# Performance work log

Measured on AMD Instinct MI355X. Metric: run time of the kernel, lower is better.

The kernel has to match this reference:

```python
import jax, jax.numpy as jnp
import numpy as np

B, T, I, H = 64, 2048, 128, 256


def setup_inputs() -> dict:
    key = jax.random.key(0)
    k1, k2, k3 = jax.random.split(key, 3)
    inputs = jax.random.normal(k1, (B, T, I), dtype=jnp.float32)
    # 4 gates (input, forget, context, output), each an affine op on [x_t, h]
    W_x = jax.random.normal(k2, (4, I, H), dtype=jnp.float32) * (1.0 / np.sqrt(I))
    W_h = jax.random.normal(k3, (4, H, H), dtype=jnp.float32) * (1.0 / np.sqrt(H))
    b = jnp.zeros((4, H), dtype=jnp.float32)
    return {"inputs": inputs, "W_x": W_x, "W_h": W_h, "b": b}


def reference(inputs, W_x, W_h, b):
    # inputs: [B, T, I]; W_x: [4, I, H]; W_h: [4, H, H]; b: [4, H]
    Bb = inputs.shape[0]
    Hh = W_h.shape[-1]
    h0 = jnp.zeros((Bb, Hh), dtype=inputs.dtype)
    c0 = jnp.zeros((Bb, Hh), dtype=inputs.dtype)

    def step(carry, x_t):
        h, c = carry
        # all 4 gate pre-activations at once: [4, B, H]
        g = (jnp.einsum('bi,gih->gbh', x_t, W_x)
             + jnp.einsum('bh,ghk->gbk', h, W_h)
             + b[:, None, :])
        i_gate = jax.nn.sigmoid(g[0])
        f_gate = jax.nn.sigmoid(g[1])
        g_gate = jnp.tanh(g[2])
        o_gate = jax.nn.sigmoid(g[3])
        c_new = f_gate * c + i_gate * g_gate
        h_new = o_gate * jnp.tanh(c_new)
        return (h_new, c_new), h_new

    xs = jnp.swapaxes(inputs, 0, 1)  # [T, B, I]
    (_, _), hs = jax.lax.scan(step, (h0, c0), xs)  # hs: [T, B, H]
    return jnp.swapaxes(hs, 0, 1)  # [B, T, H]
```

## Files before the change

kernel.cpp:

```cpp
#include <hip/hip_runtime.h>
#include <hip/hip_bf16.h>


#define B_ 64
#define T_ 2048
#define I_ 128
#define H_ 256
#define NC 1024

typedef __attribute__((ext_vector_type(8))) short bf16x8;
typedef __attribute__((ext_vector_type(4))) float f32x4;

static __device__ __forceinline__ unsigned short f2bf(float f) {
    unsigned u = __builtin_bit_cast(unsigned, f);
    u = (u + 0x7FFFu + ((u >> 16) & 1u)) >> 16;
    return (unsigned short)u;
}

static __device__ __forceinline__ int dot4(unsigned a, unsigned b, int c) {
#if __has_builtin(__builtin_amdgcn_sdot4)
    return __builtin_amdgcn_sdot4((int)a, (int)b, c, false);
#else
    int r = c;
    r += (int)(signed char)(a) * (int)(signed char)(b);
    r += (int)(signed char)(a >> 8) * (int)(signed char)(b >> 8);
    r += (int)(signed char)(a >> 16) * (int)(signed char)(b >> 16);
    r += (int)(signed char)(a >> 24) * (int)(signed char)(b >> 24);
    return r;
#endif
}

static __device__ __forceinline__ float fastrcp(float x) {
    return __builtin_amdgcn_rcpf(x);
}

__global__ void pack_wh(const float* __restrict__ Wh, unsigned* __restrict__ wq,
                        float* __restrict__ sws) {
    int col = blockIdx.x;
    int g = col >> 8, j = col & 255;
    int lane = threadIdx.x;
    float v[4];
    float m = 0.f;
#pragma unroll
    for (int u = 0; u < 4; ++u) {
        int k = lane * 4 + u;
        v[u] = Wh[(g * H_ + k) * H_ + j];
        m = fmaxf(m, fabsf(v[u]));
    }
#pragma unroll
    for (int off = 32; off; off >>= 1) m = fmaxf(m, __shfl_xor(m, off));
    float mm = (m > 0.f) ? m : 1.f;
    float inv = 127.f / mm;
    unsigned pack = 0;
#pragma unroll
    for (int u = 0; u < 4; ++u) {
        int q = (int)rintf(v[u] * inv);
        q = max(-127, min(127, q));
        pack |= ((unsigned)(q & 255)) << (8 * u);
    }
    wq[col * 64 + lane] = pack;
    if (lane == 0) sws[col] = mm / (127.f * 127.f);
}

__global__ void pack_wx(const float* __restrict__ Wx,
                        unsigned short* __restrict__ bxp) {
    int f = blockIdx.x * blockDim.x + threadIdx.x;
    int j = f & 7;
    int col = (f >> 3) & 1023;
    int c16 = f >> 13;
    int k = (c16 >> 2) * 32 + (c16 & 3) * 8 + j;
    int g = col >> 8, h = col & 255;
    bxp[f] = f2bf(Wx[(g * I_ + k) * H_ + h]);
}

__global__ __launch_bounds__(256) void gemm_gx(
    const float* __restrict__ A, const unsigned short* __restrict__ Bp,
    unsigned short* __restrict__ Cg) {
    __shared__ uint4 sm[4096];
    int tid = threadIdx.x;
    int mt = blockIdx.x, nt = blockIdx.y;

    const float* Ab = A + (size_t)mt * 128 * I_;
    unsigned* dstA = (unsigned*)sm;
#pragma unroll
    for (int it = 0; it < 16; ++it) {
        int flat = it * 1024 + tid * 4;
        float4 a4 = *(const float4*)(Ab + flat);
        int m = flat >> 7, k0 = flat & 127;
        int c16 = k0 >> 3, j0 = k0 & 7;
        unsigned lo = (unsigned)f2bf(a4.x) | ((unsigned)f2bf(a4.y) << 16);
        unsigned hi = (unsigned)f2bf(a4.z) | ((unsigned)f2bf(a4.w) << 16);
        int didx = ((c16 * 128 + m) * 16 + j0 * 2) >> 2;
        dstA[didx] = lo;
        dstA[didx + 1] = hi;
    }
    const uint4* Bq = (const uint4*)Bp;
#pragma unroll
    for (int it = 0; it < 8; ++it) {
        int chunk = it * 2 + (tid >> 7);
        int inner = tid & 127;
        sm[2048 + chunk * 128 + inner] = Bq[chunk * 1024 + nt * 128 + inner];
    }
    __syncthreads();

    int wid = tid >> 6, lane = tid & 63;
    int r = lane & 15, q = lane >> 4;
    int mw = (wid & 1) * 64, nw = (wid >> 1) * 64;
    f32x4 acc[4][4] = {};
#pragma unroll
    for (int ki = 0; ki < 4; ++ki) {
        bf16x8 af[4], bfr[4];
#pragma unroll
        for (int x = 0; x < 4; ++x) {
            af[x] = __builtin_bit_cast(bf16x8,
                                       sm[(ki * 4 + q) * 128 + mw + x * 16 + r]);
            bfr[x] = __builtin_bit_cast(
                bf16x8, sm[2048 + (ki * 4 + q) * 128 + nw + x * 16 + r]);
        }
#pragma unroll
        for (int x = 0; x < 4; ++x)
#pragma unroll
            for (int y = 0; y < 4; ++y)
                acc[x][y] = __builtin_amdgcn_mfma_f32_16x16x32_bf16(
                    af[x], bfr[y], acc[x][y], 0, 0, 0);
    }
    __syncthreads();

    _Float16* ct = (_Float16*)sm;
#pragma unroll
    for (int x = 0; x < 4; ++x)
#pragma unroll
        for (int y = 0; y < 4; ++y)
#pragma unroll
            for (int g2 = 0; g2 < 4; ++g2) {
                int row = mw + x * 16 + q * 4 + g2;
                int colc = nw + y * 16 + r;
                ct[row * 128 + colc] = (_Float16)acc[x][y][g2];
            }
    __syncthreads();
    int m = tid >> 1, half = tid & 1;
    const uint4* src = (const uint4*)sm;
    uint4* dstg =
        (uint4*)(Cg + ((size_t)(mt * 128 + m) * NC + nt * 128 + half * 64));
#pragma unroll
    for (int i = 0; i < 8; ++i) dstg[i] = src[m * 16 + half * 8 + i];
}

__global__ __launch_bounds__(1024, 4) void lstm_rec(
    const unsigned short* __restrict__ gx, const uint4* __restrict__ wq4,
    const float* __restrict__ sws, const float* __restrict__ bias,
    float* __restrict__ out) {
    int b = blockIdx.x, tid = threadIdx.x;
    int w = tid >> 6;
    int lane = tid & 63;
    int g = lane >> 4;
    int jj = lane & 15;
    int j = w * 16 + jj;
    int col = g * H_ + j;

    uint4 wv[16];
#pragma unroll
    for (int i = 0; i < 16; ++i) wv[i] = wq4[col * 16 + i];
    float sc = sws[col];
    float bb = bias[col];

    __shared__ uint4 hq[2][16];
    if (tid < 16) hq[0][tid] = (uint4){0u, 0u, 0u, 0u};
    __syncthreads();

    float c = 0.f;
    const _Float16* gxh = (const _Float16*)gx;
    size_t rowbase = (size_t)b * T_;
    float gxv = (float)gxh[rowbase * NC + col];

    for (int t = 0; t < T_; ++t) {
        size_t row = rowbase + t;
        size_t prow = rowbase + ((t < T_ - 1) ? (t + 1) : t);
        float nxv = (float)gxh[prow * NC + col];

        const uint4* hb = hq[t & 1];
        int a0 = 0, a1 = 0, a2 = 0, a3 = 0;
#pragma unroll
        for (int ib = 0; ib < 4; ++ib) {
            uint4 h0 = hb[ib * 4 + 0], h1 = hb[ib * 4 + 1];
            uint4 h2 = hb[ib * 4 + 2], h3 = hb[ib * 4 + 3];
            uint4 w0 = wv[ib * 4 + 0], w1 = wv[ib * 4 + 1];
            uint4 w2 = wv[ib * 4 + 2], w3 = wv[ib * 4 + 3];
            a0 = dot4(w0.x, h0.x, a0); a0 = dot4(w0.y, h0.y, a0);
            a0 = dot4(w0.z, h0.z, a0); a0 = dot4(w0.w, h0.w, a0);
            a1 = dot4(w1.x, h1.x, a1); a1 = dot4(w1.y, h1.y, a1);
            a1 = dot4(w1.z, h1.z, a1); a1 = dot4(w1.w, h1.w, a1);
            a2 = dot4(w2.x, h2.x, a2); a2 = dot4(w2.y, h2.y, a2);
            a2 = dot4(w2.z, h2.z, a2); a2 = dot4(w2.w, h2.w, a2);
            a3 = dot4(w3.x, h3.x, a3); a3 = dot4(w3.y, h3.y, a3);
            a3 = dot4(w3.z, h3.z, a3); a3 = dot4(w3.w, h3.w, a3);
        }
        float gpre = (float)((a0 + a1) + (a2 + a3)) * sc + gxv + bb;

        bool isg = (g == 2);
        float arg = isg ? (-2.f * gpre) : (-gpre);
        float e = __expf(arg);
        float r = fastrcp(1.f + e);
        float v = isg ? (2.f * r - 1.f) : r;

        float fv = __shfl(v, jj + 16, 64);
        float gv = __shfl(v, jj + 32, 64);
        float ov = __shfl(v, jj + 48, 64);

        if (g == 0) {
            c = fv * c + v * gv;
            float ec = __expf(-2.f * c);
            float th = 2.f * fastrcp(1.f + ec) - 1.f;
            float h = ov * th;
            out[row * H_ + j] = h;
            int qv = (int)rintf(h * 127.f);
            ((signed char*)hq[(t + 1) & 1])[j] = (signed char)qv;
        }
        __syncthreads();

        gxv = nxv;
    }
}

extern "C" void kernel_launch(void* const* d_in, const int* in_sizes, int n_in,
                              void* d_out, int out_size, void* d_ws,
                              size_t ws_size, hipStream_t stream) {
    const float* inputs = (const float*)d_in[0];
    const float* Wx = (const float*)d_in[1];
    const float* Wh = (const float*)d_in[2];
    const float* bias = (const float*)d_in[3];
    float* out = (float*)d_out;

    char* ws = (char*)d_ws;
    unsigned short* gxbuf = (unsigned short*)ws;
    size_t off = (size_t)B_ * T_ * NC * 2;
    unsigned* wq = (unsigned*)(ws + off);
    off += (size_t)NC * 64 * 4;
    float* sws = (float*)(ws + off);
    off += (size_t)NC * 4;
    unsigned short* bxp = (unsigned short*)(ws + off);
    off += (size_t)I_ * NC * 2;

    pack_wh<<<NC, 64, 0, stream>>>(Wh, wq, sws);
    pack_wx<<<(I_ * NC) / 256, 256, 0, stream>>>(Wx, bxp);
    gemm_gx<<<dim3((B_ * T_) / 128, NC / 128), 256, 0, stream>>>(inputs, bxp,
                                                                 gxbuf);
    lstm_rec<<<B_, 1024, 0, stream>>>(gxbuf, (const uint4*)wq, sws, bias, out);
}
```

Before: 2.292 ms.

## Compute recurrent int8 matvec with MFMA i8 instructions instead of sdot4

Repacks the quantized recurrent weights into the MFMA A-fragment layout. Each wave now computes its four gates' 16 hidden units with 16x16x64 int8 MFMAs, with the h vector broadcast as the B operand. Results are extracted from column 0 through a per-wave LDS scratch and read back per lane. This replaces 64 scalar dot4 ops per lane per step with a few matrix instructions, at the cost of redundant columns and an extra LDS round trip on the serial critical path.

```diff
diff --git a/kernel.cpp b/kernel.cpp
--- a/kernel.cpp
+++ b/kernel.cpp
@@ -10,6 +10,7 @@
 
 typedef __attribute__((ext_vector_type(8))) short bf16x8;
 typedef __attribute__((ext_vector_type(4))) float f32x4;
+typedef __attribute__((ext_vector_type(4))) int i32x4;
 
 static __device__ __forceinline__ unsigned short f2bf(float f) {
     unsigned u = __builtin_bit_cast(unsigned, f);
@@ -17,24 +18,11 @@
     return (unsigned short)u;
 }
 
-static __device__ __forceinline__ int dot4(unsigned a, unsigned b, int c) {
-#if __has_builtin(__builtin_amdgcn_sdot4)
-    return __builtin_amdgcn_sdot4((int)a, (int)b, c, false);
-#else
-    int r = c;
-    r += (int)(signed char)(a) * (int)(signed char)(b);
-    r += (int)(signed char)(a >> 8) * (int)(signed char)(b >> 8);
-    r += (int)(signed char)(a >> 16) * (int)(signed char)(b >> 16);
-    r += (int)(signed char)(a >> 24) * (int)(signed char)(b >> 24);
-    return r;
-#endif
-}
-
 static __device__ __forceinline__ float fastrcp(float x) {
     return __builtin_amdgcn_rcpf(x);
 }
 
-__global__ void pack_wh(const float* __restrict__ Wh, unsigned* __restrict__ wq,
+__global__ void pack_wh(const float* __restrict__ Wh, unsigned* __restrict__ afr,
                         float* __restrict__ sws) {
     int col = blockIdx.x;
     int g = col >> 8, j = col & 255;
@@ -58,7 +46,10 @@
         q = max(-127, min(127, q));
         pack |= ((unsigned)(q & 255)) << (8 * u);
     }
-    wq[col * 64 + lane] = pack;
+    int fragid = ((j >> 4) * 4 + g) * 4 + (lane >> 4);
+    int fl = (((lane & 15) >> 2) * 16) + (j & 15);
+    int didx = (fragid * 64 + fl) * 4 + (lane & 3);
+    afr[didx] = pack;
     if (lane == 0) sws[col] = mm / (127.f * 127.f);
 }
 
@@ -147,7 +138,7 @@
 }
 
 __global__ __launch_bounds__(1024, 4) void lstm_rec(
-    const unsigned short* __restrict__ gx, const uint4* __restrict__ wq4,
+    const unsigned short* __restrict__ gx, const uint4* __restrict__ afr,
     const float* __restrict__ sws, const float* __restrict__ bias,
     float* __restrict__ out) {
     int b = blockIdx.x, tid = threadIdx.x;
@@ -158,13 +149,18 @@
     int j = w * 16 + jj;
     int col = g * H_ + j;
 
-    uint4 wv[16];
-#pragma unroll
-    for (int i = 0; i < 16; ++i) wv[i] = wq4[col * 16 + i];
+    uint4 af[4][4];
+#pragma unroll
+    for (int gg = 0; gg < 4; ++gg)
+#pragma unroll
+        for (int kt = 0; kt < 4; ++kt)
+            af[gg][kt] = afr[(((w * 4 + gg) * 4) + kt) * 64 + lane];
+
     float sc = sws[col];
     float bb = bias[col];
 
     __shared__ uint4 hq[2][16];
+    __shared__ __align__(16) int sg[16 * 64];
     if (tid < 16) hq[0][tid] = (uint4){0u, 0u, 0u, 0u};
     __syncthreads();
 
@@ -178,24 +174,32 @@
         size_t prow = rowbase + ((t < T_ - 1) ? (t + 1) : t);
         float nxv = (float)gxh[prow * NC + col];
 
-        const uint4* hb = hq[t & 1];
-        int a0 = 0, a1 = 0, a2 = 0, a3 = 0;
-#pragma unroll
-        for (int ib = 0; ib < 4; ++ib) {
-            uint4 h0 = hb[ib * 4 + 0], h1 = hb[ib * 4 + 1];
-            uint4 h2 = hb[ib * 4 + 2], h3 = hb[ib * 4 + 3];
-            uint4 w0 = wv[ib * 4 + 0], w1 = wv[ib * 4 + 1];
-            uint4 w2 = wv[ib * 4 + 2], w3 = wv[ib * 4 + 3];
-            a0 = dot4(w0.x, h0.x, a0); a0 = dot4(w0.y, h0.y, a0);
-            a0 = dot4(w0.z, h0.z, a0); a0 = dot4(w0.w, h0.w, a0);
-            a1 = dot4(w1.x, h1.x, a1); a1 = dot4(w1.y, h1.y, a1);
-            a1 = dot4(w1.z, h1.z, a1); a1 = dot4(w1.w, h1.w, a1);
-            a2 = dot4(w2.x, h2.x, a2); a2 = dot4(w2.y, h2.y, a2);
-            a2 = dot4(w2.z, h2.z, a2); a2 = dot4(w2.w, h2.w, a2);
-            a3 = dot4(w3.x, h3.x, a3); a3 = dot4(w3.y, h3.y, a3);
-            a3 = dot4(w3.z, h3.z, a3); a3 = dot4(w3.w, h3.w, a3);
-        }
-        float gpre = (float)((a0 + a1) + (a2 + a3)) * sc + gxv + bb;
+        const char* hb = (const char*)hq[t & 1];
+        i32x4 d0 = {0, 0, 0, 0}, d1 = {0, 0, 0, 0};
+        i32x4 d2 = {0, 0, 0, 0}, d3 = {0, 0, 0, 0};
+#pragma unroll
+        for (int kt = 0; kt < 4; ++kt) {
+            uint4 bf = *(const uint4*)(hb + kt * 64 + ((lane >> 4) << 4));
+            i32x4 bfi = __builtin_bit_cast(i32x4, bf);
+            d0 = __builtin_amdgcn_mfma_i32_16x16x64_i8(
+                __builtin_bit_cast(i32x4, af[0][kt]), bfi, d0, 0, 0, 0);
+            d1 = __builtin_amdgcn_mfma_i32_16x16x64_i8(
+                __builtin_bit_cast(i32x4, af[1][kt]), bfi, d1, 0, 0, 0);
+            d2 = __builtin_amdgcn_mfma_i32_16x16x64_i8(
+                __builtin_bit_cast(i32x4, af[2][kt]), bfi, d2, 0, 0, 0);
+            d3 = __builtin_amdgcn_mfma_i32_16x16x64_i8(
+                __builtin_bit_cast(i32x4, af[3][kt]), bfi, d3, 0, 0, 0);
+        }
+        if ((lane & 15) == 0) {
+            int base = w * 64 + (lane >> 4) * 4;
+            *(i32x4*)&sg[base + 0 * 16] = d0;
+            *(i32x4*)&sg[base + 1 * 16] = d1;
+            *(i32x4*)&sg[base + 2 * 16] = d2;
+            *(i32x4*)&sg[base + 3 * 16] = d3;
+        }
+        __builtin_amdgcn_sched_barrier(0);
+        int gi = sg[w * 64 + lane];
+        float gpre = (float)gi * sc + gxv + bb;
 
         bool isg = (g == 2);
         float arg = isg ? (-2.f * gpre) : (-gpre);
@@ -234,16 +238,16 @@
     char* ws = (char*)d_ws;
     unsigned short* gxbuf = (unsigned short*)ws;
     size_t off = (size_t)B_ * T_ * NC * 2;
-    unsigned* wq = (unsigned*)(ws + off);
+    unsigned* afr = (unsigned*)(ws + off);
     off += (size_t)NC * 64 * 4;
     float* sws = (float*)(ws + off);
     off += (size_t)NC * 4;
     unsigned short* bxp = (unsigned short*)(ws + off);
     off += (size_t)I_ * NC * 2;
 
-    pack_wh<<<NC, 64, 0, stream>>>(Wh, wq, sws);
+    pack_wh<<<NC, 64, 0, stream>>>(Wh, afr, sws);
     pack_wx<<<(I_ * NC) / 256, 256, 0, stream>>>(Wx, bxp);
     gemm_gx<<<dim3((B_ * T_) / 128, NC / 128), 256, 0, stream>>>(inputs, bxp,
                                                                  gxbuf);
-    lstm_rec<<<B_, 1024, 0, stream>>>(gxbuf, (const uint4*)wq, sws, bias, out);
-}
+    lstm_rec<<<B_, 1024, 0, stream>>>(gxbuf, (const uint4*)afr, sws, bias, out);
+}
```

Measured after the change: 2.470 ms. +7.8%, slower.
